# Performance work log

Hardware: AMD Instinct MI355X
Metric: run time of the kernel (lower is better)

Reference implementation:

```python
import jax, jax.numpy as jnp
import numpy as np

N_ATOMS = 100000
N_BONDS = 250000
MAX_NB = 6
HIDDEN = 256
DEPTH = 3
NUM_MOLS = 2000
ATOM_FDIM = 133
BOND_FDIM = 147


def setup_inputs() -> dict:
    key = jax.random.key(0)
    ks = jax.random.split(key, 12)
    return {
        "f_atoms": jax.random.normal(ks[0], (N_ATOMS, ATOM_FDIM), jnp.float32),
        "f_bonds": jax.random.normal(ks[1], (N_BONDS, BOND_FDIM), jnp.float32),
        "w_atoms": jax.random.uniform(ks[2], (N_ATOMS,), jnp.float32),
        "w_bonds": jax.random.uniform(ks[3], (N_BONDS,), jnp.float32),
        "W_i": jax.random.normal(ks[4], (BOND_FDIM, HIDDEN), jnp.float32) * 0.05,
        "W_h": jax.random.normal(ks[5], (HIDDEN, HIDDEN), jnp.float32) * 0.05,
        "W_o": jax.random.normal(ks[6], (ATOM_FDIM + HIDDEN, HIDDEN), jnp.float32) * 0.05,
        "b_o": jnp.zeros((HIDDEN,), jnp.float32),
        "degree_of_polym": jax.random.uniform(ks[7], (NUM_MOLS,), jnp.float32),
        "a2b": jax.random.randint(ks[8], (N_ATOMS, MAX_NB), 0, N_BONDS, jnp.int32),
        "b2a": jax.random.randint(ks[9], (N_BONDS,), 0, N_ATOMS, jnp.int32),
        "b2revb": jax.random.randint(ks[10], (N_BONDS,), 0, N_BONDS, jnp.int32),
        "mol_ids": jnp.sort(jax.random.randint(ks[11], (N_ATOMS,), 0, NUM_MOLS, jnp.int32)),
    }


def reference(f_atoms, f_bonds, w_atoms, w_bonds, W_i, W_h, W_o, b_o,
              degree_of_polym, a2b, b2a, b2revb, mol_ids):
    # input-layer: bond features -> hidden messages
    inp = f_bonds @ W_i                      # [n_bonds, H]
    message = jax.nn.relu(inp)

    for _ in range(DEPTH - 1):
        # gather incoming bond messages per atom and weight them
        nei_msg = message[a2b]               # [n_atoms, max_nb, H]
        nei_w = w_bonds[a2b]                 # [n_atoms, max_nb]
        a_message = (nei_msg * nei_w[..., None]).sum(axis=1)  # [n_atoms, H]
        # directed message: total at source atom minus reverse bond
        message = a_message[b2a] - message[b2revb]             # [n_bonds, H]
        message = jax.nn.relu(inp + message @ W_h)             # dropout p=0 (eval)

    # final atom-level readout
    nei_msg = message[a2b] * w_bonds[a2b][..., None]
    a_message = nei_msg.sum(axis=1)                            # [n_atoms, H]
    a_input = jnp.concatenate([f_atoms, a_message], axis=1)    # [n_atoms, atom_fdim+H]
    atom_hiddens = jax.nn.relu(a_input @ W_o + b_o)            # [n_atoms, H]

    # per-molecule weighted mean aggregation (a_scope loop -> segment_sum)
    weighted = atom_hiddens * w_atoms[:, None]
    mol_sum = jax.ops.segment_sum(weighted, mol_ids, num_segments=NUM_MOLS)
    w_sum = jax.ops.segment_sum(w_atoms, mol_ids, num_segments=NUM_MOLS)
    safe_w = jnp.where(w_sum > 0, w_sum, 1.0)
    mol_vecs = jnp.where((w_sum > 0)[:, None], mol_sum / safe_w[:, None], 0.0)
    mol_vecs = degree_of_polym[:, None] * mol_vecs             # [num_mols, H]
    return mol_vecs
```

## Files before the change

kernel.cpp:

```cpp
#include <hip/hip_runtime.h>
#include <hip/hip_bf16.h>

typedef unsigned short u16;
typedef __bf16 bf16x8v __attribute__((ext_vector_type(8)));
typedef float f32x4v __attribute__((ext_vector_type(4)));
typedef float f32x4u __attribute__((ext_vector_type(4))) __attribute__((aligned(4)));

__device__ __forceinline__ float bf2f(u16 u) {
    union { float f; unsigned int i; } c; c.i = ((unsigned int)u) << 16; return c.f;
}
__device__ __forceinline__ u16 f2bf(float f) {
    union { float f; unsigned int i; } c; c.f = f;
    unsigned int i = c.i;
    unsigned int lsb = (i >> 16) & 1u;
    i += 0x7fffu + lsb;
    return (u16)(i >> 16);
}
__device__ __forceinline__ float lo16(unsigned u) { return bf2f((u16)(u & 0xffff)); }
__device__ __forceinline__ float hi16(unsigned u) { return bf2f((u16)(u >> 16)); }
__device__ __forceinline__ unsigned pack2(float lo, float hi) {
    return (unsigned)f2bf(lo) | ((unsigned)f2bf(hi) << 16);
}

__device__ __forceinline__ bf16x8v load_cvt8(const float* __restrict__ rowp, int k, int kmax) {
    union { unsigned u[4]; bf16x8v v; } r;
#pragma unroll
    for (int g = 0; g < 2; ++g) {
        int kk = k + g * 4;
        float f0, f1, f2, f3;
        if (kk + 3 < kmax) {
            f32x4u q = *(const f32x4u*)(rowp + kk);
            f0 = q.x; f1 = q.y; f2 = q.z; f3 = q.w;
        } else {
            f0 = (kk + 0 < kmax) ? rowp[kk + 0] : 0.f;
            f1 = (kk + 1 < kmax) ? rowp[kk + 1] : 0.f;
            f2 = (kk + 2 < kmax) ? rowp[kk + 2] : 0.f;
            f3 = (kk + 3 < kmax) ? rowp[kk + 3] : 0.f;
        }
        r.u[g * 2]     = pack2(f0, f1);
        r.u[g * 2 + 1] = pack2(f2, f3);
    }
    return r.v;
}

__global__ void pack_w(const float* __restrict__ W, u16* __restrict__ Wt, int K, int Kpad) {
    int idx = blockIdx.x * 256 + threadIdx.x;
    if (idx >= 256 * Kpad) return;
    int n = idx / Kpad, k = idx % Kpad;
    float v = (k < K) ? W[k * 256 + n] : 0.f;
    Wt[idx] = f2bf(v);
}

__global__ void pack_wo(const float* __restrict__ W_o, u16* __restrict__ Wt) {
    int idx = blockIdx.x * 256 + threadIdx.x;
    if (idx >= 256 * 448) return;
    int n = idx / 448, k = idx % 448;
    float v;
    if (k < 256)       v = W_o[(133 + k) * 256 + n];
    else if (k < 389)  v = W_o[(k - 256) * 256 + n];
    else               v = 0.f;
    Wt[idx] = f2bf(v);
}

template <bool RELU>
__global__ __launch_bounds__(256)
void gather16(const u16* __restrict__ msg, const int* __restrict__ a2b,
              const float* __restrict__ w_bonds, u16* __restrict__ out, int nAtoms) {
    int t = threadIdx.x;
    int atom = blockIdx.x * 8 + (t >> 5);
    int co = (t & 31) * 8;
    if (atom >= nAtoms) return;
    float a[8] = {0.f, 0.f, 0.f, 0.f, 0.f, 0.f, 0.f, 0.f};
#pragma unroll
    for (int j = 0; j < 6; ++j) {
        int b = a2b[atom * 6 + j];
        float w = w_bonds[b];
        uint4 v = *(const uint4*)(msg + (size_t)b * 256 + co);
        unsigned p[4] = {v.x, v.y, v.z, v.w};
#pragma unroll
        for (int q = 0; q < 4; ++q) {
            float m0 = lo16(p[q]), m1 = hi16(p[q]);
            if (RELU) { m0 = fmaxf(m0, 0.f); m1 = fmaxf(m1, 0.f); }
            a[q * 2]     += w * m0;
            a[q * 2 + 1] += w * m1;
        }
    }
    uint4 o;
    o.x = pack2(a[0], a[1]); o.y = pack2(a[2], a[3]);
    o.z = pack2(a[4], a[5]); o.w = pack2(a[6], a[7]);
    *(uint4*)(out + (size_t)atom * 256 + co) = o;
}

__global__ __launch_bounds__(512, 2)
void gemm_in(const float* __restrict__ A, const u16* __restrict__ Bt, int M,
             u16* __restrict__ out0) {
    constexpr int KPAD = 160, KMAX = 147, ASTR = 147;
    constexpr int LSTR = KPAD + 8;
    __shared__ u16 Bs[256 * LSTR];
    const int tid = threadIdx.x;
    const int wave = tid >> 6;
    const int lane = tid & 63;
    const int mrow = lane & 15;
    const int quad = lane >> 4;

    constexpr int KC = KPAD / 8;
    for (int i = tid; i < 256 * KC; i += 512) {
        int r = i / KC, kc = i % KC;
        *(uint4*)&Bs[r * LSTR + kc * 8] = *(const uint4*)&Bt[(size_t)r * KPAD + kc * 8];
    }
    __syncthreads();

    for (long chunk = blockIdx.x; chunk * 256 < (long)M; chunk += gridDim.x) {
        const long mbase = chunk * 256 + wave * 32;
        const float* rowp[2];
#pragma unroll
        for (int t = 0; t < 2; ++t) {
            long r = mbase + t * 16 + mrow;
            if (r >= M) r = M - 1;
            rowp[t] = A + r * ASTR;
        }

        f32x4v acc[2][16];
#pragma unroll
        for (int t = 0; t < 2; ++t)
#pragma unroll
            for (int j = 0; j < 16; ++j) acc[t][j] = (f32x4v){0.f, 0.f, 0.f, 0.f};

#pragma unroll 2
        for (int k0 = 0; k0 < KPAD; k0 += 32) {
            bf16x8v a_frag[2];
#pragma unroll
            for (int t = 0; t < 2; ++t)
                a_frag[t] = load_cvt8(rowp[t], k0 + quad * 8, KMAX);
#pragma unroll
            for (int jg = 0; jg < 4; ++jg) {
                bf16x8v b_frag[4];
#pragma unroll
                for (int j4 = 0; j4 < 4; ++j4)
                    b_frag[j4] = *(const bf16x8v*)&Bs[((jg * 4 + j4) * 16 + mrow) * LSTR + k0 + quad * 8];
#pragma unroll
                for (int t = 0; t < 2; ++t)
#pragma unroll
                    for (int j4 = 0; j4 < 4; ++j4)
                        acc[t][jg * 4 + j4] = __builtin_amdgcn_mfma_f32_16x16x32_bf16(
                            a_frag[t], b_frag[j4], acc[t][jg * 4 + j4], 0, 0, 0);
            }
        }

#pragma unroll
        for (int t = 0; t < 2; ++t)
#pragma unroll
            for (int r = 0; r < 4; ++r) {
                long grow = mbase + t * 16 + quad * 4 + r;
                if (grow < M)
#pragma unroll
                    for (int j = 0; j < 16; ++j)
                        out0[(size_t)grow * 256 + j * 16 + mrow] = f2bf(acc[t][j][r]);
            }
    }
}

template <bool RELUV>
__global__ __launch_bounds__(512, 2)
void gemm_mp(const u16* __restrict__ amsg, const u16* __restrict__ msgsrc,
             const int* __restrict__ b2a, const int* __restrict__ b2revb,
             const u16* __restrict__ Bt, int M,
             const u16* __restrict__ inp, u16* __restrict__ out0) {
    constexpr int KPAD = 256;
    constexpr int LSTR = KPAD + 8;
    __shared__ u16 Bs[256 * LSTR];
    const int tid = threadIdx.x;
    const int wave = tid >> 6;
    const int lane = tid & 63;
    const int mrow = lane & 15;
    const int quad = lane >> 4;

    constexpr int KC = KPAD / 8;
    for (int i = tid; i < 256 * KC; i += 512) {
        int r = i / KC, kc = i % KC;
        *(uint4*)&Bs[r * LSTR + kc * 8] = *(const uint4*)&Bt[(size_t)r * KPAD + kc * 8];
    }
    __syncthreads();

    for (long chunk = blockIdx.x; chunk * 256 < (long)M; chunk += gridDim.x) {
        const long mbase = chunk * 256 + wave * 32;
        size_t soff[2], roff[2];
#pragma unroll
        for (int t = 0; t < 2; ++t) {
            long b = mbase + t * 16 + mrow;
            if (b >= M) b = M - 1;
            soff[t] = (size_t)b2a[b] * 256 + quad * 8;
            roff[t] = (size_t)b2revb[b] * 256 + quad * 8;
        }

        f32x4v acc[2][16];
#pragma unroll
        for (int t = 0; t < 2; ++t)
#pragma unroll
            for (int j = 0; j < 16; ++j) acc[t][j] = (f32x4v){0.f, 0.f, 0.f, 0.f};

#pragma unroll 2
        for (int k0 = 0; k0 < KPAD; k0 += 32) {
            bf16x8v a_frag[2];
#pragma unroll
            for (int t = 0; t < 2; ++t) {
                uint4 va = *(const uint4*)&amsg[soff[t] + k0];
                uint4 vr = *(const uint4*)&msgsrc[roff[t] + k0];
                unsigned pa[4] = {va.x, va.y, va.z, va.w};
                unsigned pr[4] = {vr.x, vr.y, vr.z, vr.w};
                union { unsigned u[4]; bf16x8v v; } res;
#pragma unroll
                for (int p = 0; p < 4; ++p) {
                    float rl = lo16(pr[p]), rh = hi16(pr[p]);
                    if (RELUV) { rl = fmaxf(rl, 0.f); rh = fmaxf(rh, 0.f); }
                    res.u[p] = pack2(lo16(pa[p]) - rl, hi16(pa[p]) - rh);
                }
                a_frag[t] = res.v;
            }
#pragma unroll
            for (int jg = 0; jg < 4; ++jg) {
                bf16x8v b_frag[4];
#pragma unroll
                for (int j4 = 0; j4 < 4; ++j4)
                    b_frag[j4] = *(const bf16x8v*)&Bs[((jg * 4 + j4) * 16 + mrow) * LSTR + k0 + quad * 8];
#pragma unroll
                for (int t = 0; t < 2; ++t)
#pragma unroll
                    for (int j4 = 0; j4 < 4; ++j4)
                        acc[t][jg * 4 + j4] = __builtin_amdgcn_mfma_f32_16x16x32_bf16(
                            a_frag[t], b_frag[j4], acc[t][jg * 4 + j4], 0, 0, 0);
            }
        }

#pragma unroll
        for (int t = 0; t < 2; ++t)
#pragma unroll
            for (int r = 0; r < 4; ++r) {
                long grow = mbase + t * 16 + quad * 4 + r;
                if (grow < M)
#pragma unroll
                    for (int j = 0; j < 16; ++j) {
                        size_t idx = (size_t)grow * 256 + j * 16 + mrow;
                        float s = bf2f(inp[idx]) + acc[t][j][r];
                        out0[idx] = f2bf(s > 0.f ? s : 0.f);
                    }
            }
    }
}

__global__ __launch_bounds__(512, 2)
void gemm_ro(const u16* __restrict__ A1, const float* __restrict__ A2,
             const u16* __restrict__ Bt, int M,
             const float* __restrict__ bias, float* __restrict__ outf) {
    constexpr int KPAD = 448, KSPLIT = 256, K2 = 192, KMAX2 = 133;
    constexpr int LSTR = KPAD + 8;
    constexpr int NROWS = 128;
    __shared__ u16 Bs[NROWS * LSTR];
    const int tid = threadIdx.x;
    const int wave = tid >> 6;
    const int lane = tid & 63;
    const int mrow = lane & 15;
    const int quad = lane >> 4;
    const int nbase = blockIdx.y * NROWS;

    constexpr int KC = KPAD / 8;
    for (int i = tid; i < NROWS * KC; i += 512) {
        int r = i / KC, kc = i % KC;
        *(uint4*)&Bs[r * LSTR + kc * 8] =
            *(const uint4*)&Bt[(size_t)(nbase + r) * KPAD + kc * 8];
    }
    __syncthreads();

    for (long chunk = blockIdx.x; chunk * 256 < (long)M; chunk += gridDim.x) {
        const long mbase = chunk * 256 + wave * 32;
        long row[2];
#pragma unroll
        for (int t = 0; t < 2; ++t) {
            long r = mbase + t * 16 + mrow;
            if (r >= M) r = M - 1;
            row[t] = r;
        }

        f32x4v acc[2][8];
#pragma unroll
        for (int t = 0; t < 2; ++t)
#pragma unroll
            for (int j = 0; j < 8; ++j) acc[t][j] = (f32x4v){0.f, 0.f, 0.f, 0.f};

#pragma unroll 2
        for (int k0 = 0; k0 < KSPLIT; k0 += 32) {
            bf16x8v a_frag[2], b_frag[8];
#pragma unroll
            for (int t = 0; t < 2; ++t)
                a_frag[t] = *(const bf16x8v*)&A1[row[t] * KSPLIT + k0 + quad * 8];
#pragma unroll
            for (int j = 0; j < 8; ++j)
                b_frag[j] = *(const bf16x8v*)&Bs[(j * 16 + mrow) * LSTR + k0 + quad * 8];
#pragma unroll
            for (int t = 0; t < 2; ++t)
#pragma unroll
                for (int j = 0; j < 8; ++j)
                    acc[t][j] = __builtin_amdgcn_mfma_f32_16x16x32_bf16(
                        a_frag[t], b_frag[j], acc[t][j], 0, 0, 0);
        }
#pragma unroll 2
        for (int k0 = 0; k0 < K2; k0 += 32) {
            bf16x8v a_frag[2], b_frag[8];
#pragma unroll
            for (int t = 0; t < 2; ++t)
                a_frag[t] = load_cvt8(A2 + row[t] * KMAX2, k0 + quad * 8, KMAX2);
#pragma unroll
            for (int j = 0; j < 8; ++j)
                b_frag[j] = *(const bf16x8v*)&Bs[(j * 16 + mrow) * LSTR + KSPLIT + k0 + quad * 8];
#pragma unroll
            for (int t = 0; t < 2; ++t)
#pragma unroll
                for (int j = 0; j < 8; ++j)
                    acc[t][j] = __builtin_amdgcn_mfma_f32_16x16x32_bf16(
                        a_frag[t], b_frag[j], acc[t][j], 0, 0, 0);
        }

#pragma unroll
        for (int t = 0; t < 2; ++t)
#pragma unroll
            for (int r = 0; r < 4; ++r) {
                long grow = mbase + t * 16 + quad * 4 + r;
                if (grow < M)
#pragma unroll
                    for (int j = 0; j < 8; ++j) {
                        int gcol = nbase + j * 16 + mrow;
                        float s = acc[t][j][r] + bias[gcol];
                        outf[(size_t)grow * 256 + gcol] = s > 0.f ? s : 0.f;
                    }
            }
    }
}

__global__ __launch_bounds__(256)
void aggregate_kernel(const float* __restrict__ hid, const float* __restrict__ w_atoms,
                      const int* __restrict__ mol_ids, const float* __restrict__ deg,
                      float* __restrict__ out, int nAtoms) {
    int m = blockIdx.x;
    int t = threadIdx.x;
    int lo = 0, hi = nAtoms;
    while (lo < hi) { int mid = (lo + hi) >> 1; if (mol_ids[mid] < m) lo = mid + 1; else hi = mid; }
    int start = lo;
    lo = start; hi = nAtoms;
    while (lo < hi) { int mid = (lo + hi) >> 1; if (mol_ids[mid] < m + 1) lo = mid + 1; else hi = mid; }
    int end = lo;
    float acc = 0.f, wsum = 0.f;
    for (int a = start; a < end; ++a) {
        float w = w_atoms[a];
        wsum += w;
        acc += w * hid[(size_t)a * 256 + t];
    }
    float res = (wsum > 0.f) ? deg[m] * acc / wsum : 0.f;
    out[m * 256 + t] = res;
}

extern "C" void kernel_launch(void* const* d_in, const int* in_sizes, int n_in,
                              void* d_out, int out_size, void* d_ws, size_t ws_size,
                              hipStream_t stream) {
    const float* f_atoms = (const float*)d_in[0];
    const float* f_bonds = (const float*)d_in[1];
    const float* w_atoms = (const float*)d_in[2];
    const float* w_bonds = (const float*)d_in[3];
    const float* W_i     = (const float*)d_in[4];
    const float* W_h     = (const float*)d_in[5];
    const float* W_o     = (const float*)d_in[6];
    const float* b_o     = (const float*)d_in[7];
    const float* deg     = (const float*)d_in[8];
    const int*   a2b     = (const int*)d_in[9];
    const int*   b2a     = (const int*)d_in[10];
    const int*   b2revb  = (const int*)d_in[11];
    const int*   mol_ids = (const int*)d_in[12];
    float* out = (float*)d_out;

    const int nB = 250000, nA = 100000, nM = 2000;

    char* ws = (char*)d_ws;
    u16* inp    = (u16*)(ws);
    u16* msgA   = (u16*)(ws + 128000000L);
    float* hid  = (float*)(ws + 256000000L);
    u16* amsg   = (u16*)(ws + 384000000L);
    u16* wt_i   = (u16*)(ws + 435200000L);
    u16* wt_h   = (u16*)(ws + 435200000L + 81920L);
    u16* wt_o   = (u16*)(ws + 435200000L + 81920L + 131072L);

    if (ws_size < 435642368UL) return;

    dim3 b256(256), b512(512);
    pack_w<<<dim3((256 * 160 + 255) / 256), b256, 0, stream>>>(W_i, wt_i, 147, 160);
    pack_w<<<dim3((256 * 256 + 255) / 256), b256, 0, stream>>>(W_h, wt_h, 256, 256);
    pack_wo<<<dim3((256 * 448 + 255) / 256), b256, 0, stream>>>(W_o, wt_o);

    gemm_in<<<dim3(977), b512, 0, stream>>>(f_bonds, wt_i, nB, inp);

    gather16<true><<<dim3(nA / 8), b256, 0, stream>>>(inp, a2b, w_bonds, amsg, nA);
    gemm_mp<true><<<dim3(977), b512, 0, stream>>>(
        amsg, inp, b2a, b2revb, wt_h, nB, inp, msgA);

    gather16<false><<<dim3(nA / 8), b256, 0, stream>>>(msgA, a2b, w_bonds, amsg, nA);
    gemm_mp<false><<<dim3(977), b512, 0, stream>>>(
        amsg, msgA, b2a, b2revb, wt_h, nB, inp, inp);

    gather16<false><<<dim3(nA / 8), b256, 0, stream>>>(inp , a2b, w_bonds, amsg, nA);
    gemm_ro<<<dim3(391, 2), b512, 0, stream>>>(amsg, f_atoms, wt_o, nA, b_o, hid);

    aggregate_kernel<<<dim3(nM), b256, 0, stream>>>(hid, w_atoms, mol_ids, deg, out, nA);
}
```

Measured before the change: 852.0 us.

## Split message-passing GEMM over output columns and fold subtraction into MFMAs

gemm_mp now splits the 256 output columns across two blocks via blockIdx.y. That halves the shared-memory weight tile and the accumulator registers, and the launch bound rises to 4 blocks per CU to raise occupancy. The bf16 unpack/subtract/repack of the gathered atom message and the reverse-bond message is replaced by a sign-bit flip (with a bitwise ReLU for the first layer). The product is then computed as two accumulated MFMAs, A·W plus (−R)·W. This trades the VALU conversion work for twice the MFMA count, and each A row is gathered by both column blocks.

```diff
diff --git a/kernel.cpp b/kernel.cpp
--- a/kernel.cpp
+++ b/kernel.cpp
@@ -20,6 +20,13 @@
 __device__ __forceinline__ float hi16(unsigned u) { return bf2f((u16)(u >> 16)); }
 __device__ __forceinline__ unsigned pack2(float lo, float hi) {
     return (unsigned)f2bf(lo) | ((unsigned)f2bf(hi) << 16);
+}
+
+__device__ __forceinline__ unsigned neg2(unsigned u) { return u ^ 0x80008000u; }
+__device__ __forceinline__ unsigned relu_neg2(unsigned u) {
+    unsigned s = u & 0x80008000u;
+    unsigned m = (s - (s >> 15)) | s;
+    return (u ^ 0x80008000u) & ~m;
 }
 
 __device__ __forceinline__ bf16x8v load_cvt8(const float* __restrict__ rowp, int k, int kmax) {
@@ -161,24 +168,26 @@
 }
 
 template <bool RELUV>
-__global__ __launch_bounds__(512, 2)
+__global__ __launch_bounds__(512, 4)
 void gemm_mp(const u16* __restrict__ amsg, const u16* __restrict__ msgsrc,
              const int* __restrict__ b2a, const int* __restrict__ b2revb,
              const u16* __restrict__ Bt, int M,
              const u16* __restrict__ inp, u16* __restrict__ out0) {
     constexpr int KPAD = 256;
     constexpr int LSTR = KPAD + 8;
-    __shared__ u16 Bs[256 * LSTR];
+    constexpr int NROWS = 128;
+    __shared__ u16 Bs[NROWS * LSTR];
     const int tid = threadIdx.x;
     const int wave = tid >> 6;
     const int lane = tid & 63;
     const int mrow = lane & 15;
     const int quad = lane >> 4;
+    const int nbase = blockIdx.y * NROWS;
 
     constexpr int KC = KPAD / 8;
-    for (int i = tid; i < 256 * KC; i += 512) {
+    for (int i = tid; i < NROWS * KC; i += 512) {
         int r = i / KC, kc = i % KC;
-        *(uint4*)&Bs[r * LSTR + kc * 8] = *(const uint4*)&Bt[(size_t)r * KPAD + kc * 8];
+        *(uint4*)&Bs[r * LSTR + kc * 8] = *(const uint4*)&Bt[(size_t)(nbase + r) * KPAD + kc * 8];
     }
     __syncthreads();
 
@@ -193,32 +202,32 @@
             roff[t] = (size_t)b2revb[b] * 256 + quad * 8;
         }
 
-        f32x4v acc[2][16];
-#pragma unroll
-        for (int t = 0; t < 2; ++t)
-#pragma unroll
-            for (int j = 0; j < 16; ++j) acc[t][j] = (f32x4v){0.f, 0.f, 0.f, 0.f};
+        f32x4v acc[2][8];
+#pragma unroll
+        for (int t = 0; t < 2; ++t)
+#pragma unroll
+            for (int j = 0; j < 8; ++j) acc[t][j] = (f32x4v){0.f, 0.f, 0.f, 0.f};
 
 #pragma unroll 2
         for (int k0 = 0; k0 < KPAD; k0 += 32) {
-            bf16x8v a_frag[2];
+            bf16x8v a1[2], a2[2];
 #pragma unroll
             for (int t = 0; t < 2; ++t) {
-                uint4 va = *(const uint4*)&amsg[soff[t] + k0];
+                union { uint4 q; bf16x8v v; } ua, ur;
+                ua.q = *(const uint4*)&amsg[soff[t] + k0];
                 uint4 vr = *(const uint4*)&msgsrc[roff[t] + k0];
-                unsigned pa[4] = {va.x, va.y, va.z, va.w};
-                unsigned pr[4] = {vr.x, vr.y, vr.z, vr.w};
-                union { unsigned u[4]; bf16x8v v; } res;
-#pragma unroll
-                for (int p = 0; p < 4; ++p) {
-                    float rl = lo16(pr[p]), rh = hi16(pr[p]);
-                    if (RELUV) { rl = fmaxf(rl, 0.f); rh = fmaxf(rh, 0.f); }
-                    res.u[p] = pack2(lo16(pa[p]) - rl, hi16(pa[p]) - rh);
+                if (RELUV) {
+                    ur.q.x = relu_neg2(vr.x); ur.q.y = relu_neg2(vr.y);
+                    ur.q.z = relu_neg2(vr.z); ur.q.w = relu_neg2(vr.w);
+                } else {
+                    ur.q.x = neg2(vr.x); ur.q.y = neg2(vr.y);
+                    ur.q.z = neg2(vr.z); ur.q.w = neg2(vr.w);
                 }
-                a_frag[t] = res.v;
-            }
-#pragma unroll
-            for (int jg = 0; jg < 4; ++jg) {
+                a1[t] = ua.v;
+                a2[t] = ur.v;
+            }
+#pragma unroll
+            for (int jg = 0; jg < 2; ++jg) {
                 bf16x8v b_frag[4];
 #pragma unroll
                 for (int j4 = 0; j4 < 4; ++j4)
@@ -226,9 +235,12 @@
 #pragma unroll
                 for (int t = 0; t < 2; ++t)
 #pragma unroll
-                    for (int j4 = 0; j4 < 4; ++j4)
+                    for (int j4 = 0; j4 < 4; ++j4) {
                         acc[t][jg * 4 + j4] = __builtin_amdgcn_mfma_f32_16x16x32_bf16(
-                            a_frag[t], b_frag[j4], acc[t][jg * 4 + j4], 0, 0, 0);
+                            a1[t], b_frag[j4], acc[t][jg * 4 + j4], 0, 0, 0);
+                        acc[t][jg * 4 + j4] = __builtin_amdgcn_mfma_f32_16x16x32_bf16(
+                            a2[t], b_frag[j4], acc[t][jg * 4 + j4], 0, 0, 0);
+                    }
             }
         }
 
@@ -239,8 +251,8 @@
                 long grow = mbase + t * 16 + quad * 4 + r;
                 if (grow < M)
 #pragma unroll
-                    for (int j = 0; j < 16; ++j) {
-                        size_t idx = (size_t)grow * 256 + j * 16 + mrow;
+                    for (int j = 0; j < 8; ++j) {
+                        size_t idx = (size_t)grow * 256 + nbase + j * 16 + mrow;
                         float s = bf2f(inp[idx]) + acc[t][j][r];
                         out0[idx] = f2bf(s > 0.f ? s : 0.f);
                     }
@@ -397,11 +409,11 @@
     gemm_in<<<dim3(977), b512, 0, stream>>>(f_bonds, wt_i, nB, inp);
 
     gather16<true><<<dim3(nA / 8), b256, 0, stream>>>(inp, a2b, w_bonds, amsg, nA);
-    gemm_mp<true><<<dim3(977), b512, 0, stream>>>(
+    gemm_mp<true><<<dim3(977, 2), b512, 0, stream>>>(
         amsg, inp, b2a, b2revb, wt_h, nB, inp, msgA);
 
     gather16<false><<<dim3(nA / 8), b256, 0, stream>>>(msgA, a2b, w_bonds, amsg, nA);
-    gemm_mp<false><<<dim3(977), b512, 0, stream>>>(
+    gemm_mp<false><<<dim3(977, 2), b512, 0, stream>>>(
         amsg, msgA, b2a, b2revb, wt_h, nB, inp, inp);
 
     gather16<false><<<dim3(nA / 8), b256, 0, stream>>>(inp , a2b, w_bonds, amsg, nA);
```

Result: slower. 894.7 us (+5.0%).
